# Kernel tuning notes

Measured on AMD Instinct MI355X. Metric: run time of the kernel, lower is better.

## Reference

```python
import jax, jax.numpy as jnp
import numpy as np
from jax import lax

NL, HID, DIN, DST, DCONV, DTR = 4, 256, 512, 16, 4, 16  # layers, d_model, expand*d_model, d_state, d_conv, dt_rank
B, H, W = 4, 256, 256


def setup_inputs() -> dict:
    key = jax.random.key(0)
    ks = jax.random.split(key, 8)
    def n(k, s, sc=0.02):
        return jax.random.normal(k, s, dtype=jnp.float32) * sc
    return {
        "x": jax.random.normal(ks[0], (B, 3, H, W), dtype=jnp.float32),
        "conv1_w": n(ks[1], (HID // 2, 3, 3, 3), 0.1), "conv1_b": jnp.zeros((HID // 2,), jnp.float32),
        "gn1_w": jnp.ones((HID // 2,), jnp.float32), "gn1_b": jnp.zeros((HID // 2,), jnp.float32),
        "conv2_w": n(ks[2], (HID, HID // 2, 3, 3), 0.05), "conv2_b": jnp.zeros((HID,), jnp.float32),
        "gn2_w": jnp.ones((HID,), jnp.float32), "gn2_b": jnp.zeros((HID,), jnp.float32),
        "ln_w": jnp.ones((NL, HID), jnp.float32), "ln_b": jnp.zeros((NL, HID), jnp.float32),
        "in_proj_w": n(ks[3], (NL, 2 * DIN, HID)),
        "conv1d_w": n(ks[4], (NL, DIN, 1, DCONV), 0.1), "conv1d_b": jnp.zeros((NL, DIN), jnp.float32),
        "x_proj_w": n(ks[5], (NL, DTR + 2 * DST, DIN)),
        "dt_proj_w": n(ks[6], (NL, DIN, DTR), 0.1),
        "dt_proj_b": jnp.full((NL, DIN), -4.6, dtype=jnp.float32),  # softplus(-4.6) ~ 0.01
        "A_log": jnp.broadcast_to(jnp.log(jnp.arange(1, DST + 1, dtype=jnp.float32)), (NL, DIN, DST)) + jnp.zeros((NL, DIN, DST), jnp.float32),
        "D": jnp.ones((NL, DIN), jnp.float32),
        "out_proj_w": n(ks[7], (NL, HID, DIN)),
    }


def conv2d_s2(x, w, b):
    y = lax.conv_general_dilated(x, w, (2, 2), [(1, 1), (1, 1)],
                                 dimension_numbers=('NCHW', 'OIHW', 'NCHW'))
    return y + b[None, :, None, None]


def group_norm(x, w, b, groups=8, eps=1e-5):
    Bb, C, Hh, Ww = x.shape
    xg = x.reshape(Bb, groups, C // groups, Hh, Ww)
    m = xg.mean((2, 3, 4), keepdims=True)
    v = xg.var((2, 3, 4), keepdims=True)
    xg = (xg - m) * lax.rsqrt(v + eps)
    return xg.reshape(Bb, C, Hh, Ww) * w[None, :, None, None] + b[None, :, None, None]


def layer_norm(x, w, b, eps=1e-5):
    m = x.mean(-1, keepdims=True)
    v = x.var(-1, keepdims=True)
    return (x - m) * lax.rsqrt(v + eps) * w + b


def mamba(x, ipw, cw, cb, xpw, dpw, dpb, A_log, Dp, opw):
    # x: [B, L, HID]
    Bb, L, _ = x.shape
    xz = jnp.einsum('bld,ed->ble', x, ipw)           # [B, L, 2*DIN]
    xc, z = jnp.split(xz, 2, axis=-1)
    # depthwise causal conv1d over L
    u = xc.transpose(0, 2, 1)                        # [B, DIN, L]
    u = lax.conv_general_dilated(u, cw, (1,), [(DCONV - 1, 0)],
                                 dimension_numbers=('NCH', 'OIH', 'NCH'),
                                 feature_group_count=DIN)
    xc = jax.nn.silu(u + cb[None, :, None]).transpose(0, 2, 1)  # [B, L, DIN]
    x_dbl = jnp.einsum('bld,ed->ble', xc, xpw)       # [B, L, DTR+2*DST]
    dt, Bm, Cm = jnp.split(x_dbl, [DTR, DTR + DST], axis=-1)
    delta = jax.nn.softplus(jnp.einsum('blr,dr->bld', dt, dpw) + dpb)  # [B, L, DIN]
    A = -jnp.exp(A_log)                              # [DIN, DST]
    dA = jnp.exp(jnp.einsum('bld,dn->bldn', delta, A))
    dBu = jnp.einsum('bld,bln,bld->bldn', delta, Bm, xc)

    def step(h, inp):
        dA_t, dBu_t, C_t = inp
        h = dA_t * h + dBu_t                         # [B, DIN, DST]
        return h, jnp.einsum('bdn,bn->bd', h, C_t)

    h0 = jnp.zeros((Bb, DIN, DST), x.dtype)
    _, ys = lax.scan(step, h0, (dA.transpose(1, 0, 2, 3), dBu.transpose(1, 0, 2, 3), Cm.transpose(1, 0, 2)))
    y = ys.transpose(1, 0, 2) + xc * Dp              # [B, L, DIN]
    y = y * jax.nn.silu(z)
    return jnp.einsum('bld,ed->ble', y, opw)         # [B, L, HID]


def reference(x, conv1_w, conv1_b, gn1_w, gn1_b, conv2_w, conv2_b, gn2_w, gn2_b,
              ln_w, ln_b, in_proj_w, conv1d_w, conv1d_b, x_proj_w, dt_proj_w,
              dt_proj_b, A_log, D, out_proj_w):
    y = jax.nn.silu(group_norm(conv2d_s2(x, conv1_w, conv1_b), gn1_w, gn1_b))
    y = jax.nn.silu(group_norm(conv2d_s2(y, conv2_w, conv2_b), gn2_w, gn2_b))
    Bb, C, h, w = y.shape
    s = y.reshape(Bb, C, h * w).transpose(0, 2, 1)   # b (h w) c
    for i in range(NL):
        s = s + mamba(layer_norm(s, ln_w[i], ln_b[i]), in_proj_w[i], conv1d_w[i],
                      conv1d_b[i], x_proj_w[i], dt_proj_w[i], dt_proj_b[i],
                      A_log[i], D[i], out_proj_w[i])
    return (s, h, w)
```

## Files before the change

### kernel.cpp

```cpp
#include <hip/hip_runtime.h>
#include <math.h>

#define BB 4
#define C1 128
#define H1 128
#define W1 128
#define C2 256
#define H2 64
#define W2 64
#define LSEQ 4096
#define HID 256
#define DIN 512
#define DST 16
#define DTR 16
#define NL 4
#define NCHUNK 128
#define LCH 32

typedef unsigned short u16;
using short8 = __attribute__((ext_vector_type(8))) short;
using f32x4  = __attribute__((ext_vector_type(4))) float;
using f32x2  = __attribute__((ext_vector_type(2))) float;

static __device__ __forceinline__ float dsilu(float x){
    return x / (1.0f + __expf(-x));
}
static __device__ __forceinline__ u16 f2bf(float f){
    unsigned u = __float_as_uint(f);
    u += 0x7FFF + ((u >> 16) & 1);
    return (u16)(u >> 16);
}
static __device__ __forceinline__ float bf2f(u16 v){
    return __uint_as_float(((unsigned)v) << 16);
}

#define GLL16(g, l) __builtin_amdgcn_global_load_lds( \
    (const __attribute__((address_space(1))) void*)(g), \
    (__attribute__((address_space(3))) void*)(l), 16, 0, 0)

__global__ void f2bf_kernel(const float* __restrict__ src, u16* __restrict__ dst){
    int idx = blockIdx.x * 256 + threadIdx.x;
    dst[idx] = f2bf(src[idx]);
}
__global__ void wdt_prep_kernel(const float* __restrict__ xpw, const float* __restrict__ dpw,
                                u16* __restrict__ wcomb){
    int idx = blockIdx.x * 256 + threadIdx.x;
    int k = idx & 511;
    int n = (idx >> 9) % 640;
    int layer = idx / (640*512);
    u16 val = 0;
    if(n < 512){
        const float* dp = dpw + ((long)layer*512 + n)*16;
        const float* xp = xpw + (long)layer*48*512 + k;
        float acc = 0.f;
        #pragma unroll
        for(int r = 0; r < 16; ++r) acc = fmaf(dp[r], xp[(long)r*512], acc);
        val = f2bf(acc);
    } else if(n < 544){
        int row = n - 512 + 16;
        val = f2bf(xpw[((long)layer*48 + row)*512 + k]);
    }
    wcomb[((long)layer*640 + n)*512 + k] = val;
}
__global__ void c2w_prep_kernel(const float* __restrict__ src, u16* __restrict__ dst){
    int idx = blockIdx.x * 256 + threadIdx.x;
    int ci = idx & 127, p = (idx >> 7) % 9, co = idx / (9*128);
    int kh = p / 3, kw = p - 3*kh;
    dst[idx] = f2bf(src[((co*128 + ci)*3 + kh)*3 + kw]);
}
__global__ void xt_zero_kernel(unsigned* __restrict__ xt){
    xt[blockIdx.x * 256 + threadIdx.x] = 0;
}

__global__ __launch_bounds__(256) void conv1_kernel(
        const float* __restrict__ x, const float* __restrict__ w,
        const float* __restrict__ bias, float* __restrict__ y){
    __shared__ float xs[9][260];
    int oh = blockIdx.x, b = blockIdx.y;
    int tid = threadIdx.x;
    #pragma unroll
    for(int r = 0; r < 9; ++r){
        int ci = r / 3, kh = r - 3*ci;
        int ih = 2*oh - 1 + kh;
        float v = 0.f;
        if(ih >= 0) v = x[((b*3 + ci)*256 + ih)*256 + tid];
        xs[r][tid + 1] = v;
        if(tid == 0) xs[r][0] = 0.f;
    }
    __syncthreads();
    int co = tid >> 1, h = tid & 1;
    float wr[27];
    #pragma unroll
    for(int j = 0; j < 27; ++j) wr[j] = w[co*27 + j];
    float bz = bias[co];
    long obase = ((long)((b*128 + co)*128 + oh))*128 + h*64;
    #pragma unroll 4
    for(int i = 0; i < 64; ++i){
        int iw0 = 2*(h*64 + i);
        float acc = bz;
        #pragma unroll
        for(int r = 0; r < 9; ++r){
            acc = fmaf(xs[r][iw0+0], wr[r*3+0], acc);
            acc = fmaf(xs[r][iw0+1], wr[r*3+1], acc);
            acc = fmaf(xs[r][iw0+2], wr[r*3+2], acc);
        }
        y[obase + i] = acc;
    }
}

__global__ void zero_stats_kernel(float* __restrict__ stats){
    stats[threadIdx.x] = 0.0f;
}

__global__ void gn_stats_kernel(const float* __restrict__ x, float* __restrict__ stats,
                                int elems_per_group){
    const int EPB = 16384;
    long base = (long)blockIdx.x * EPB;
    int g = (int)(base / elems_per_group);
    float s = 0.f, ss = 0.f;
    for(int j = threadIdx.x; j < EPB; j += 256){
        float v = x[base + j];
        s += v; ss += v*v;
    }
    #pragma unroll
    for(int off = 32; off; off >>= 1){
        s  += __shfl_down(s,  off);
        ss += __shfl_down(ss, off);
    }
    __shared__ float ls[4], lss[4];
    int wid = threadIdx.x >> 6, lane = threadIdx.x & 63;
    if(lane == 0){ ls[wid] = s; lss[wid] = ss; }
    __syncthreads();
    if(threadIdx.x == 0){
        atomicAdd(&stats[g],      ls[0]+ls[1]+ls[2]+ls[3]);
        atomicAdd(&stats[32+g], lss[0]+lss[1]+lss[2]+lss[3]);
    }
}

__global__ void gn1_transform_kernel(const float* __restrict__ y1, const float* __restrict__ stats,
                                     const float* __restrict__ w, const float* __restrict__ bias,
                                     u16* __restrict__ xt){
    __shared__ float tile[32][33];
    int b = blockIdx.z >> 7, ih = blockIdx.z & 127;
    int c0 = blockIdx.y * 32, w0 = blockIdx.x * 32;
    int tx = threadIdx.x, ty = threadIdx.y;
    const float cnt = 16.f * 128.f * 128.f;
    #pragma unroll
    for(int i = 0; i < 4; ++i){
        int ci = c0 + ty + i*8;
        int g = b*8 + (ci >> 4);
        float mean = stats[g] / cnt;
        float var  = stats[32+g] / cnt - mean*mean;
        float rstd = rsqrtf(var + 1e-5f);
        float v = y1[(((long)(b*C1 + ci))*H1 + ih)*W1 + w0 + tx];
        tile[ty + i*8][tx] = dsilu((v - mean) * rstd * w[ci] + bias[ci]);
    }
    __syncthreads();
    #pragma unroll
    for(int i = 0; i < 4; ++i){
        int iwl = ty + i*8;
        xt[((long)(b*130 + ih + 1)*130 + (w0 + iwl + 1))*128 + c0 + tx] = f2bf(tile[tx][iwl]);
    }
}

__global__ __launch_bounds__(256) void conv2gemm_bf16_kernel(
        const u16* __restrict__ xt, const u16* __restrict__ w2,
        const float* __restrict__ bias, float* __restrict__ y2t){
    __shared__ u16 Asm[128*32];
    __shared__ u16 Bsm[128*32];
    int m0 = blockIdx.x * 128, n0 = blockIdx.y * 128;
    int tid = threadIdx.x;
    long abase[2]; const u16* bbase[2];
    #pragma unroll
    for(int it = 0; it < 2; ++it){
        int c = it*256 + tid;
        int r = c >> 2, q = (c & 3) * 8;
        int m = m0 + r;
        int b = m >> 12, oh = (m >> 6) & 63, ow = m & 63;
        abase[it] = ((long)(b*130 + 2*oh)*130 + 2*ow)*128 + q;
        bbase[it] = w2 + (long)(n0 + r)*1152 + q;
    }
    int wave = tid >> 6, lane = tid & 63;
    int wr = wave >> 1, wc = wave & 1;
    int lm = lane & 15, lq = lane >> 4;
    f32x4 acc[4][4] = {};
    #pragma unroll 1
    for(int p = 0; p < 9; ++p){
        int kh = p / 3, kw = p - 3*kh;
        int aoff = (kh*130 + kw)*128;
        #pragma unroll 1
        for(int ci0 = 0; ci0 < 128; ci0 += 32){
            #pragma unroll
            for(int it = 0; it < 2; ++it){
                int c = it*256 + tid;
                GLL16(xt + abase[it] + aoff + ci0, &Asm[c*8]);
                GLL16(bbase[it] + p*128 + ci0, &Bsm[c*8]);
            }
            __syncthreads();
            short8 af[4], bf[4];
            #pragma unroll
            for(int i = 0; i < 4; ++i){
                af[i] = *(const short8*)&Asm[(wr*64 + i*16 + lm)*32 + lq*8];
                bf[i] = *(const short8*)&Bsm[(wc*64 + i*16 + lm)*32 + lq*8];
            }
            #pragma unroll
            for(int i = 0; i < 4; ++i)
                #pragma unroll
                for(int j = 0; j < 4; ++j)
                    acc[i][j] = __builtin_amdgcn_mfma_f32_16x16x32_bf16(af[i], bf[j], acc[i][j], 0, 0, 0);
            __syncthreads();
        }
    }
    #pragma unroll
    for(int i = 0; i < 4; ++i){
        long row = m0 + wr*64 + i*16 + lq*4;
        #pragma unroll
        for(int j = 0; j < 4; ++j){
            int col = n0 + wc*64 + j*16 + lm;
            float bz = bias[col];
            #pragma unroll
            for(int r = 0; r < 4; ++r)
                y2t[(row + r)*256L + col] = acc[i][j][r] + bz;
        }
    }
}

__global__ void gn2t_stats_kernel(const float* __restrict__ y2t, float* __restrict__ stats){
    int b = blockIdx.y;
    long row0 = (long)b*LSEQ + blockIdx.x*64;
    int c = threadIdx.x;
    float s = 0.f, ss = 0.f;
    for(int r = 0; r < 64; ++r){
        float v = y2t[(row0 + r)*C2 + c];
        s += v; ss += v*v;
    }
    #pragma unroll
    for(int off = 16; off; off >>= 1){
        s  += __shfl_down(s,  off);
        ss += __shfl_down(ss, off);
    }
    if((c & 31) == 0){
        int g = b*8 + (c >> 5);
        atomicAdd(&stats[g], s);
        atomicAdd(&stats[32+g], ss);
    }
}

__global__ void gn2t_apply_ln_kernel(const float* __restrict__ y2t, const float* __restrict__ stats,
                                     const float* __restrict__ gw, const float* __restrict__ gb,
                                     const float* __restrict__ lw, const float* __restrict__ lb,
                                     float* __restrict__ s, u16* __restrict__ xln){
    long row = blockIdx.x;
    int c = threadIdx.x;
    int b = (int)(row >> 12);
    int g = b*8 + (c >> 5);
    const float cnt = 32.f * (float)LSEQ;
    float mean = stats[g] / cnt;
    float var  = stats[32+g] / cnt - mean*mean;
    float rstd = rsqrtf(var + 1e-5f);
    float v = dsilu((y2t[row*HID + c] - mean) * rstd * gw[c] + gb[c]);
    s[row*HID + c] = v;
    float sm = v, sq = v*v;
    #pragma unroll
    for(int off = 32; off; off >>= 1){
        sm += __shfl_down(sm, off);
        sq += __shfl_down(sq, off);
    }
    __shared__ float pa[4], pb[4], res[2];
    int wid = c >> 6, lane = c & 63;
    if(lane == 0){ pa[wid] = sm; pb[wid] = sq; }
    __syncthreads();
    if(c == 0){
        float t  = pa[0]+pa[1]+pa[2]+pa[3];
        float tt = pb[0]+pb[1]+pb[2]+pb[3];
        float m2 = t / 256.f;
        float v2 = tt / 256.f - m2*m2;
        res[0] = m2; res[1] = rsqrtf(v2 + 1e-5f);
    }
    __syncthreads();
    xln[row*HID + c] = f2bf((v - res[0]) * res[1] * lw[c] + lb[c]);
}

__global__ __launch_bounds__(256) void gemm_bf16_kernel(
        const u16* __restrict__ A, const u16* __restrict__ B, void* __restrict__ Cv,
        int K, int Nact, int ldc, int mode){
    __shared__ u16 Asm[128*32];
    __shared__ u16 Bsm[128*32];
    int m0 = blockIdx.x * 128, n0 = blockIdx.y * 128;
    int tid = threadIdx.x;
    int wave = tid >> 6, lane = tid & 63;
    int wr = wave >> 1, wc = wave & 1;
    int lm = lane & 15, lq = lane >> 4;
    f32x4 acc[4][4] = {};
    for(int k0 = 0; k0 < K; k0 += 32){
        #pragma unroll
        for(int it = 0; it < 2; ++it){
            int c = it*256 + tid;
            int row = c >> 2, kq = (c & 3) * 8;
            GLL16(A + (long)(m0 + row)*K + k0 + kq, &Asm[c*8]);
            GLL16(B + (long)(n0 + row)*K + k0 + kq, &Bsm[c*8]);
        }
        __syncthreads();
        short8 af[4], bf[4];
        #pragma unroll
        for(int i = 0; i < 4; ++i){
            af[i] = *(const short8*)&Asm[(wr*64 + i*16 + lm)*32 + lq*8];
            bf[i] = *(const short8*)&Bsm[(wc*64 + i*16 + lm)*32 + lq*8];
        }
        #pragma unroll
        for(int i = 0; i < 4; ++i)
            #pragma unroll
            for(int j = 0; j < 4; ++j)
                acc[i][j] = __builtin_amdgcn_mfma_f32_16x16x32_bf16(af[i], bf[j], acc[i][j], 0, 0, 0);
        __syncthreads();
    }
    #pragma unroll
    for(int i = 0; i < 4; ++i){
        long row = m0 + wr*64 + i*16 + lq*4;
        #pragma unroll
        for(int j = 0; j < 4; ++j){
            int col = n0 + wc*64 + j*16 + lm;
            if(col < Nact){
                #pragma unroll
                for(int r = 0; r < 4; ++r){
                    long idx = (row + r)*(long)ldc + col;
                    if(mode == 2) ((u16*)Cv)[idx] = f2bf(acc[i][j][r]);
                    else          ((float*)Cv)[idx] = acc[i][j][r];
                }
            }
        }
    }
}

__global__ __launch_bounds__(256) void gemm_dtbc_kernel(
        const u16* __restrict__ A, const u16* __restrict__ B,
        const float* __restrict__ dpb, u16* __restrict__ dv,
        float* __restrict__ xdbl32){
    __shared__ u16 Asm[128*32];
    __shared__ u16 Bsm[128*32];
    int m0 = blockIdx.x * 128, n0 = blockIdx.y * 128;
    int tid = threadIdx.x;
    int wave = tid >> 6, lane = tid & 63;
    int wr = wave >> 1, wc = wave & 1;
    int lm = lane & 15, lq = lane >> 4;
    f32x4 acc[4][4] = {};
    for(int k0 = 0; k0 < 512; k0 += 32){
        #pragma unroll
        for(int it = 0; it < 2; ++it){
            int c = it*256 + tid;
            int row = c >> 2, kq = (c & 3) * 8;
            GLL16(A + (long)(m0 + row)*512 + k0 + kq, &Asm[c*8]);
            GLL16(B + (long)(n0 + row)*512 + k0 + kq, &Bsm[c*8]);
        }
        __syncthreads();
        short8 af[4], bf[4];
        #pragma unroll
        for(int i = 0; i < 4; ++i){
            af[i] = *(const short8*)&Asm[(wr*64 + i*16 + lm)*32 + lq*8];
            bf[i] = *(const short8*)&Bsm[(wc*64 + i*16 + lm)*32 + lq*8];
        }
        #pragma unroll
        for(int i = 0; i < 4; ++i)
            #pragma unroll
            for(int j = 0; j < 4; ++j)
                acc[i][j] = __builtin_amdgcn_mfma_f32_16x16x32_bf16(af[i], bf[j], acc[i][j], 0, 0, 0);
        __syncthreads();
    }
    if(n0 < 512){
        #pragma unroll
        for(int i = 0; i < 4; ++i){
            long row = m0 + wr*64 + i*16 + lq*4;
            #pragma unroll
            for(int j = 0; j < 4; ++j){
                int col = n0 + wc*64 + j*16 + lm;
                float bz = dpb[col];
                #pragma unroll
                for(int r = 0; r < 4; ++r){
                    float v = acc[i][j][r] + bz;
                    v = (v > 20.f) ? v : __logf(1.f + __expf(v));
                    dv[(row + r)*512L + col] = f2bf(v);
                }
            }
        }
    } else {
        #pragma unroll
        for(int i = 0; i < 4; ++i){
            long row = m0 + wr*64 + i*16 + lq*4;
            #pragma unroll
            for(int j = 0; j < 4; ++j){
                int lcol = wc*64 + j*16 + lm;
                if(lcol < 32){
                    #pragma unroll
                    for(int r = 0; r < 4; ++r)
                        xdbl32[(row + r)*32L + lcol] = acc[i][j][r];
                }
            }
        }
    }
}

__global__ __launch_bounds__(256) void gemm_out_ln_kernel(
        const u16* __restrict__ A, const u16* __restrict__ B,
        float* __restrict__ s, u16* __restrict__ xln,
        const float* __restrict__ lw, const float* __restrict__ lb){
    __shared__ u16 Asm[64*32];
    __shared__ u16 Bsm[256*32];
    int m0 = blockIdx.x * 64;
    int tid = threadIdx.x;
    int w = tid >> 6, lane = tid & 63;
    int lm = lane & 15, lq = lane >> 4;
    f32x4 acc[16] = {};
    for(int k0 = 0; k0 < 512; k0 += 32){
        {
            int row = tid >> 2, kq = (tid & 3) * 8;
            GLL16(A + (long)(m0 + row)*512 + k0 + kq, &Asm[tid*8]);
        }
        #pragma unroll
        for(int it = 0; it < 4; ++it){
            int c = it*256 + tid;
            int row = c >> 2, kq = (c & 3) * 8;
            GLL16(B + (long)row*512 + k0 + kq, &Bsm[c*8]);
        }
        __syncthreads();
        short8 af = *(const short8*)&Asm[(w*16 + lm)*32 + lq*8];
        #pragma unroll
        for(int j = 0; j < 16; ++j){
            short8 bf = *(const short8*)&Bsm[(j*16 + lm)*32 + lq*8];
            acc[j] = __builtin_amdgcn_mfma_f32_16x16x32_bf16(af, bf, acc[j], 0, 0, 0);
        }
        __syncthreads();
    }
    int row0 = m0 + w*16 + lq*4;
    float psum[4] = {0.f,0.f,0.f,0.f}, psq[4] = {0.f,0.f,0.f,0.f};
    #pragma unroll
    for(int j = 0; j < 16; ++j){
        int col = j*16 + lm;
        #pragma unroll
        for(int r = 0; r < 4; ++r){
            long idx = (long)(row0 + r)*HID + col;
            float v = s[idx] + acc[j][r];
            acc[j][r] = v;
            s[idx] = v;
            psum[r] += v; psq[r] += v*v;
        }
    }
    #pragma unroll
    for(int mask = 1; mask <= 8; mask <<= 1){
        #pragma unroll
        for(int r = 0; r < 4; ++r){
            psum[r] += __shfl_xor(psum[r], mask);
            psq[r]  += __shfl_xor(psq[r],  mask);
        }
    }
    float mean[4], rstd[4];
    #pragma unroll
    for(int r = 0; r < 4; ++r){
        mean[r] = psum[r] * (1.f/256.f);
        float var = psq[r] * (1.f/256.f) - mean[r]*mean[r];
        rstd[r] = rsqrtf(var + 1e-5f);
    }
    #pragma unroll
    for(int j = 0; j < 16; ++j){
        int col = j*16 + lm;
        float wv = lw[col], bv = lb[col];
        #pragma unroll
        for(int r = 0; r < 4; ++r){
            long idx = (long)(row0 + r)*HID + col;
            xln[idx] = f2bf((acc[j][r] - mean[r]) * rstd[r] * wv + bv);
        }
    }
}

__global__ void conv1d_silu_kernel(const u16* __restrict__ xz, const float* __restrict__ w,
                                   const float* __restrict__ bias, u16* __restrict__ xcv){
    int idx = blockIdx.x * 256 + threadIdx.x;
    int e = idx * 8;
    int d0 = e & 511;
    long m = e >> 9;
    int l = (int)(m & 4095);
    short8 xrow[4];
    const u16* xp = xz + m*(2*DIN) + d0;
    #pragma unroll
    for(int j = 0; j < 4; ++j){
        int t = l - 3 + j;
        if(t >= 0) xrow[j] = *(const short8*)(xp + (long)(j-3)*(2*DIN));
        else       xrow[j] = (short8){0,0,0,0,0,0,0,0};
    }
    float wv[8][4];
    #pragma unroll
    for(int k = 0; k < 8; k += 2){
        float4 a = *(const float4*)(w + (d0+k)*4);
        float4 b = *(const float4*)(w + (d0+k+1)*4);
        wv[k][0]=a.x; wv[k][1]=a.y; wv[k][2]=a.z; wv[k][3]=a.w;
        wv[k+1][0]=b.x; wv[k+1][1]=b.y; wv[k+1][2]=b.z; wv[k+1][3]=b.w;
    }
    float bz[8];
    {
        float4 a = *(const float4*)(bias + d0);
        float4 b = *(const float4*)(bias + d0 + 4);
        bz[0]=a.x; bz[1]=a.y; bz[2]=a.z; bz[3]=a.w;
        bz[4]=b.x; bz[5]=b.y; bz[6]=b.z; bz[7]=b.w;
    }
    short8 out;
    #pragma unroll
    for(int k = 0; k < 8; ++k){
        float acc = bz[k];
        #pragma unroll
        for(int j = 0; j < 4; ++j)
            acc = fmaf(bf2f((u16)xrow[j][k]), wv[k][j], acc);
        out[k] = (short)f2bf(dsilu(acc));
    }
    *(short8*)(xcv + m*DIN + d0) = out;
}

__global__ __launch_bounds__(256) void scan1_kernel(
        const u16* __restrict__ xcvb, const u16* __restrict__ dvin,
        const float* __restrict__ xdbl32, const float* __restrict__ Alog,
        float* __restrict__ aprod, float* __restrict__ hend){
    int d = blockIdx.y * 256 + threadIdx.x;
    int c = blockIdx.x;
    int b = blockIdx.z;
    __shared__ float bm[LCH][16];
    {
        int t = threadIdx.x >> 4, n = threadIdx.x & 15;
        #pragma unroll
        for(int it = 0; it < 2; ++it){
            long p = ((long)(b*LSEQ + c*LCH + t + it*16))*32;
            bm[t + it*16][n] = xdbl32[p + n];
        }
    }
    __syncthreads();
    float An[16];
    #pragma unroll
    for(int n = 0; n < 16; ++n)
        An[n] = -__expf(Alog[d*16 + n]);
    float An0 = An[0];
    bool structural = true;
    #pragma unroll
    for(int n = 0; n < 16; ++n)
        structural = structural && (fabsf(An[n] - (float)(n+1)*An0) <= 1e-3f*(float)(n+1));
    long base = ((long)(b*LSEQ + c*LCH))*DIN + d;
    long ob = (((long)(b*NCHUNK + c))*DIN + d)*16;
    if(structural){
        f32x2 h2[8];
        #pragma unroll
        for(int i = 0; i < 8; ++i) h2[i] = (f32x2){0.f, 0.f};
        float sumdv = 0.f;
        float xv_n = bf2f(xcvb[base]);
        float dv_n = bf2f(dvin[base]);
        for(int t = 0; t < LCH; ++t){
            float xv = xv_n, dv = dv_n;
            if(t + 1 < LCH){
                xv_n = bf2f(xcvb[base + (long)(t+1)*DIN]);
                dv_n = bf2f(dvin[base + (long)(t+1)*DIN]);
            }
            sumdv += dv;
            float db = dv * xv;
            float r1 = __expf(dv * An0);
            float r2 = r1 * r1;
            f32x2 rr = {r2, r2};
            f32x2 e2[8];
            e2[0] = (f32x2){r1, r2};
            #pragma unroll
            for(int i = 1; i < 8; ++i) e2[i] = e2[i-1] * rr;
            f32x2 db2 = {db, db};
            const f32x2* b2 = (const f32x2*)&bm[t][0];
            #pragma unroll
            for(int i = 0; i < 8; ++i) h2[i] = e2[i]*h2[i] + db2*b2[i];
        }
        float R = __expf(An0 * sumdv);
        float Rp = R;
        const float* hp = (const float*)h2;
        #pragma unroll
        for(int n = 0; n < 16; ++n){
            aprod[ob+n] = Rp; Rp *= R;
            hend[ob+n] = hp[n];
        }
    } else {
        float h[16], ap[16];
        #pragma unroll
        for(int n = 0; n < 16; ++n){ h[n] = 0.f; ap[n] = 1.f; }
        for(int t = 0; t < LCH; ++t){
            float dv = bf2f(dvin[base + (long)t*DIN]);
            float db = dv * bf2f(xcvb[base + (long)t*DIN]);
            #pragma unroll
            for(int n = 0; n < 16; ++n){
                float e = __expf(dv * An[n]);
                ap[n] *= e;
                h[n] = fmaf(e, h[n], db * bm[t][n]);
            }
        }
        #pragma unroll
        for(int n = 0; n < 16; ++n){ aprod[ob+n] = ap[n]; hend[ob+n] = h[n]; }
    }
}

__global__ void scan2_kernel(const float* __restrict__ aprod, const float* __restrict__ hend,
                             float* __restrict__ hinit){
    int idx = blockIdx.x * 256 + threadIdx.x;
    int n = idx & 15, d = (idx >> 4) & 511, b = idx >> 13;
    const long stride = (long)DIN * 16;
    long p0 = (((long)(b*NCHUNK))*DIN + d)*16 + n;
    float h = 0.f;
    for(int c = 0; c < NCHUNK; c += 8){
        float a[8], e[8];
        #pragma unroll
        for(int j = 0; j < 8; ++j){
            long p = p0 + (long)(c + j)*stride;
            a[j] = aprod[p]; e[j] = hend[p];
        }
        #pragma unroll
        for(int j = 0; j < 8; ++j){
            hinit[p0 + (long)(c + j)*stride] = h;
            h = fmaf(a[j], h, e[j]);
        }
    }
}

__global__ __launch_bounds__(256) void scan3_kernel(
        const u16* __restrict__ xcvb, const u16* __restrict__ dvin,
        const float* __restrict__ xdbl32, const float* __restrict__ Alog,
        const float* __restrict__ hinit, const float* __restrict__ Dp,
        const u16* __restrict__ xz, u16* __restrict__ yout){
    int d = blockIdx.y * 256 + threadIdx.x;
    int c = blockIdx.x;
    int b = blockIdx.z;
    __shared__ float bm[LCH][16], cm[LCH][16];
    {
        int t = threadIdx.x >> 4, n = threadIdx.x & 15;
        #pragma unroll
        for(int it = 0; it < 2; ++it){
            long p = ((long)(b*LSEQ + c*LCH + t + it*16))*32;
            bm[t + it*16][n] = xdbl32[p + n];
            cm[t + it*16][n] = xdbl32[p + 16 + n];
        }
    }
    __syncthreads();
    float An[16];
    long hb = (((long)(b*NCHUNK + c))*DIN + d)*16;
    #pragma unroll
    for(int n = 0; n < 16; ++n)
        An[n] = -__expf(Alog[d*16 + n]);
    float An0 = An[0];
    bool structural = true;
    #pragma unroll
    for(int n = 0; n < 16; ++n)
        structural = structural && (fabsf(An[n] - (float)(n+1)*An0) <= 1e-3f*(float)(n+1));
    float Dv = Dp[d];
    long base  = ((long)(b*LSEQ + c*LCH))*DIN + d;
    long zbase = ((long)(b*LSEQ + c*LCH))*(2*DIN) + DIN + d;
    if(structural){
        f32x2 h2[8];
        {
            const f32x2* hi = (const f32x2*)&hinit[hb];
            #pragma unroll
            for(int i = 0; i < 8; ++i) h2[i] = hi[i];
        }
        float xv_n = bf2f(xcvb[base]);
        float z_n  = bf2f(xz[zbase]);
        float dv_n = bf2f(dvin[base]);
        for(int t = 0; t < LCH; ++t){
            float xv = xv_n, z = z_n, dv = dv_n;
            if(t + 1 < LCH){
                xv_n = bf2f(xcvb[base + (long)(t+1)*DIN]);
                z_n  = bf2f(xz[zbase + (long)(t+1)*(2*DIN)]);
                dv_n = bf2f(dvin[base + (long)(t+1)*DIN]);
            }
            float db = dv * xv;
            float r1 = __expf(dv * An0);
            float r2 = r1 * r1;
            f32x2 rr = {r2, r2};
            f32x2 e2[8];
            e2[0] = (f32x2){r1, r2};
            #pragma unroll
            for(int i = 1; i < 8; ++i) e2[i] = e2[i-1] * rr;
            f32x2 db2 = {db, db};
            const f32x2* b2 = (const f32x2*)&bm[t][0];
            const f32x2* c2 = (const f32x2*)&cm[t][0];
            f32x2 y2 = {0.f, 0.f};
            #pragma unroll
            for(int i = 0; i < 8; ++i){
                h2[i] = e2[i]*h2[i] + db2*b2[i];
                y2 = y2 + h2[i]*c2[i];
            }
            float y = y2[0] + y2[1];
            y = fmaf(xv, Dv, y);
            yout[base + (long)t*DIN] = f2bf(y * dsilu(z));
        }
    } else {
        float h[16];
        #pragma unroll
        for(int n = 0; n < 16; ++n) h[n] = hinit[hb + n];
        for(int t = 0; t < LCH; ++t){
            float dv = bf2f(dvin[base + (long)t*DIN]);
            float xv = bf2f(xcvb[base + (long)t*DIN]);
            float db = dv * xv;
            float y = 0.f;
            #pragma unroll
            for(int n = 0; n < 16; ++n){
                float e = __expf(dv * An[n]);
                h[n] = fmaf(e, h[n], db * bm[t][n]);
                y = fmaf(h[n], cm[t][n], y);
            }
            y = fmaf(xv, Dv, y);
            float z = bf2f(xz[zbase + (long)t*(2*DIN)]);
            yout[base + (long)t*DIN] = f2bf(y * dsilu(z));
        }
    }
}

__global__ void copyout_kernel(const float* __restrict__ s, float* __restrict__ out, int out_size){
    int idx = blockIdx.x * 256 + threadIdx.x;
    if(idx >= out_size) return;
    out[idx] = (idx < BB*LSEQ*HID) ? s[idx] : 64.0f;
}

extern "C" void kernel_launch(void* const* d_in, const int* in_sizes, int n_in,
                              void* d_out, int out_size, void* d_ws, size_t ws_size,
                              hipStream_t stream){
    const float* x        = (const float*)d_in[0];
    const float* conv1_w  = (const float*)d_in[1];
    const float* conv1_b  = (const float*)d_in[2];
    const float* gn1_w    = (const float*)d_in[3];
    const float* gn1_b    = (const float*)d_in[4];
    const float* conv2_w  = (const float*)d_in[5];
    const float* conv2_b  = (const float*)d_in[6];
    const float* gn2_w    = (const float*)d_in[7];
    const float* gn2_b    = (const float*)d_in[8];
    const float* ln_w     = (const float*)d_in[9];
    const float* ln_b     = (const float*)d_in[10];
    const float* in_proj  = (const float*)d_in[11];
    const float* c1d_w    = (const float*)d_in[12];
    const float* c1d_b    = (const float*)d_in[13];
    const float* x_proj   = (const float*)d_in[14];
    const float* dt_w     = (const float*)d_in[15];
    const float* dt_b     = (const float*)d_in[16];
    const float* A_log    = (const float*)d_in[17];
    const float* Dvec     = (const float*)d_in[18];
    const float* out_proj = (const float*)d_in[19];

    float* ws = (float*)d_ws;
    float* s      = ws;
    u16*   xz_bf  = (u16*)(ws + 4194304);
    float* y1     = ws + 4194304;
    u16*   xt     = (u16*)(ws + 12582912);
    u16*   xcv_bf = (u16*)(ws + 16909312);
    float* y2t    = ws + 16909312;
    u16*   xln_bf = (u16*)(ws + 21103616);
    float* xdbl   = ws + 23200768;
    float* aprod  = ws + 23987200;
    float* hendb  = ws + 28181504;
    u16*   y_bf   = (u16*)aprod;
    float* hinit  = ws + 32375808;
    float* stats  = ws + 36570112;
    u16*   ipw_bf = (u16*)(ws + 36570176);
    u16*   opw_bf = ipw_bf + 1048576;
    u16*   c2w_bf = opw_bf + 524288;
    u16*   dv_bf  = (u16*)(ws + 37635200);
    u16*   wcomb  = (u16*)(ws + 41829504);

    f2bf_kernel<<<4096, 256, 0, stream>>>(in_proj, ipw_bf);
    f2bf_kernel<<<2048, 256, 0, stream>>>(out_proj, opw_bf);
    c2w_prep_kernel<<<1152, 256, 0, stream>>>(conv2_w, c2w_bf);
    wdt_prep_kernel<<<5120, 256, 0, stream>>>(x_proj, dt_w, wcomb);

    conv1_kernel<<<dim3(128,4), 256, 0, stream>>>(x, conv1_w, conv1_b, y1);
    zero_stats_kernel<<<1, 64, 0, stream>>>(stats);
    gn_stats_kernel<<<512, 256, 0, stream>>>(y1, stats, 16*H1*W1);
    xt_zero_kernel<<<16900, 256, 0, stream>>>((unsigned*)xt);
    gn1_transform_kernel<<<dim3(4,4,512), dim3(32,8), 0, stream>>>(y1, stats, gn1_w, gn1_b, xt);
    conv2gemm_bf16_kernel<<<dim3(128,2), 256, 0, stream>>>(xt, c2w_bf, conv2_b, y2t);
    zero_stats_kernel<<<1, 64, 0, stream>>>(stats);
    gn2t_stats_kernel<<<dim3(64,4), 256, 0, stream>>>(y2t, stats);
    gn2t_apply_ln_kernel<<<16384, 256, 0, stream>>>(y2t, stats, gn2_w, gn2_b,
                                                    ln_w, ln_b, s, xln_bf);

    for(int layer = 0; layer < NL; ++layer){
        const float* cw  = c1d_w + (long)layer*DIN*4;
        const float* cb  = c1d_b + (long)layer*DIN;
        const float* dpb = dt_b  + (long)layer*DIN;
        const float* Al  = A_log + (long)layer*DIN*DST;
        const float* Dl  = Dvec  + (long)layer*DIN;
        int lnext = (layer + 1) & 3;

        gemm_bf16_kernel<<<dim3(128,8), 256, 0, stream>>>(
            xln_bf, ipw_bf + (long)layer*1024*256, xz_bf, HID, 2*DIN, 2*DIN, 2);
        conv1d_silu_kernel<<<4096, 256, 0, stream>>>(xz_bf, cw, cb, xcv_bf);
        gemm_dtbc_kernel<<<dim3(128,5), 256, 0, stream>>>(
            xcv_bf, wcomb + (long)layer*640*512, dpb, dv_bf, xdbl);
        scan1_kernel<<<dim3(NCHUNK,2,BB), 256, 0, stream>>>(
            xcv_bf, dv_bf, xdbl, Al, aprod, hendb);
        scan2_kernel<<<128, 256, 0, stream>>>(aprod, hendb, hinit);
        scan3_kernel<<<dim3(NCHUNK,2,BB), 256, 0, stream>>>(
            xcv_bf, dv_bf, xdbl, Al, hinit, Dl, xz_bf, y_bf);
        gemm_out_ln_kernel<<<256, 256, 0, stream>>>(
            y_bf, opw_bf + (long)layer*256*512, s, xln_bf,
            ln_w + lnext*HID, ln_b + lnext*HID);
    }

    copyout_kernel<<<(out_size + 255)/256, 256, 0, stream>>>(s, (float*)d_out, out_size);
}
```

Measured before the change: 864.7 us.

## Double-buffer LDS tiles with async prefetch and XOR-swizzle in all bf16 GEMMs

Converts the four MFMA GEMM kernels (conv2 implicit GEMM, generic GEMM, dt/BC GEMM, out-proj+LN GEMM) to double-buffered LDS. The next K-tile is issued through global_load_lds while the current tile is consumed, using explicit vmcnt waits and raw barriers. It also XOR-swizzles the 16-byte chunk placement within each row to cut LDS bank conflicts on the short8 fragment reads. The cost is twice the shared memory per block, which may lower occupancy, plus reliance on hand-placed waitcnt correctness.

New measurement: 845.2 us. 1.02x faster.

```diff
diff --git a/kernel.cpp b/kernel.cpp
--- a/kernel.cpp
+++ b/kernel.cpp
@@ -38,6 +38,16 @@
     (const __attribute__((address_space(1))) void*)(g), \
     (__attribute__((address_space(3))) void*)(l), 16, 0, 0)
 
+#define VMW4 asm volatile("s_waitcnt vmcnt(4)" ::: "memory")
+#define VMW5 asm volatile("s_waitcnt vmcnt(5)" ::: "memory")
+#define VMW0 asm volatile("s_waitcnt vmcnt(0)" ::: "memory")
+
+static __device__ __forceinline__ void blockbar(){
+    asm volatile("" ::: "memory");
+    __builtin_amdgcn_s_barrier();
+    asm volatile("" ::: "memory");
+}
+
 __global__ void f2bf_kernel(const float* __restrict__ src, u16* __restrict__ dst){
     int idx = blockIdx.x * 256 + threadIdx.x;
     dst[idx] = f2bf(src[idx]);
@@ -166,50 +176,63 @@
 __global__ __launch_bounds__(256) void conv2gemm_bf16_kernel(
         const u16* __restrict__ xt, const u16* __restrict__ w2,
         const float* __restrict__ bias, float* __restrict__ y2t){
-    __shared__ u16 Asm[128*32];
-    __shared__ u16 Bsm[128*32];
+    __shared__ u16 Asm[2][128*32];
+    __shared__ u16 Bsm[2][128*32];
     int m0 = blockIdx.x * 128, n0 = blockIdx.y * 128;
     int tid = threadIdx.x;
-    long abase[2]; const u16* bbase[2];
+    long abase[2]; const u16* bbase[2]; int ldst[2];
     #pragma unroll
     for(int it = 0; it < 2; ++it){
         int c = it*256 + tid;
-        int r = c >> 2, q = (c & 3) * 8;
+        int r = c >> 2;
+        int kq = ((c & 3) ^ ((r >> 1) & 3)) * 8;
         int m = m0 + r;
         int b = m >> 12, oh = (m >> 6) & 63, ow = m & 63;
-        abase[it] = ((long)(b*130 + 2*oh)*130 + 2*ow)*128 + q;
-        bbase[it] = w2 + (long)(n0 + r)*1152 + q;
+        abase[it] = ((long)(b*130 + 2*oh)*130 + 2*ow)*128 + kq;
+        bbase[it] = w2 + (long)(n0 + r)*1152 + kq;
+        ldst[it] = c*8;
     }
     int wave = tid >> 6, lane = tid & 63;
     int wr = wave >> 1, wc = wave & 1;
     int lm = lane & 15, lq = lane >> 4;
+    int swq = (lq ^ ((lm >> 1) & 3)) * 8;
     f32x4 acc[4][4] = {};
-    #pragma unroll 1
-    for(int p = 0; p < 9; ++p){
-        int kh = p / 3, kw = p - 3*kh;
-        int aoff = (kh*130 + kw)*128;
-        #pragma unroll 1
-        for(int ci0 = 0; ci0 < 128; ci0 += 32){
+    #pragma unroll
+    for(int it = 0; it < 2; ++it){
+        GLL16(xt + abase[it], &Asm[0][ldst[it]]);
+        GLL16(bbase[it], &Bsm[0][ldst[it]]);
+    }
+    for(int kk = 0; kk < 36; ++kk){
+        int cur = kk & 1;
+        if(kk + 1 < 36){
+            int k2 = kk + 1;
+            int p = k2 >> 2, cs = k2 & 3;
+            int kh = p / 3, kw = p - 3*kh;
+            int ao = (kh*130 + kw)*128 + cs*32;
+            int bo = k2*32;
             #pragma unroll
             for(int it = 0; it < 2; ++it){
-                int c = it*256 + tid;
-                GLL16(xt + abase[it] + aoff + ci0, &Asm[c*8]);
-                GLL16(bbase[it] + p*128 + ci0, &Bsm[c*8]);
-            }
-            __syncthreads();
-            short8 af[4], bf[4];
-            #pragma unroll
-            for(int i = 0; i < 4; ++i){
-                af[i] = *(const short8*)&Asm[(wr*64 + i*16 + lm)*32 + lq*8];
-                bf[i] = *(const short8*)&Bsm[(wc*64 + i*16 + lm)*32 + lq*8];
-            }
-            #pragma unroll
-            for(int i = 0; i < 4; ++i)
-                #pragma unroll
-                for(int j = 0; j < 4; ++j)
-                    acc[i][j] = __builtin_amdgcn_mfma_f32_16x16x32_bf16(af[i], bf[j], acc[i][j], 0, 0, 0);
-            __syncthreads();
-        }
+                GLL16(xt + abase[it] + ao, &Asm[cur^1][ldst[it]]);
+                GLL16(bbase[it] + bo, &Bsm[cur^1][ldst[it]]);
+            }
+            VMW4;
+        } else {
+            VMW0;
+        }
+        blockbar();
+        short8 af[4], bf[4];
+        #pragma unroll
+        for(int i = 0; i < 4; ++i){
+            af[i] = *(const short8*)&Asm[cur][(wr*64 + i*16 + lm)*32 + swq];
+            bf[i] = *(const short8*)&Bsm[cur][(wc*64 + i*16 + lm)*32 + swq];
+        }
+        #pragma unroll
+        for(int i = 0; i < 4; ++i)
+            #pragma unroll
+            for(int j = 0; j < 4; ++j)
+                acc[i][j] = __builtin_amdgcn_mfma_f32_16x16x32_bf16(af[i], bf[j], acc[i][j], 0, 0, 0);
+        __builtin_amdgcn_sched_barrier(0);
+        blockbar();
     }
     #pragma unroll
     for(int i = 0; i < 4; ++i){
@@ -284,35 +307,58 @@
 __global__ __launch_bounds__(256) void gemm_bf16_kernel(
         const u16* __restrict__ A, const u16* __restrict__ B, void* __restrict__ Cv,
         int K, int Nact, int ldc, int mode){
-    __shared__ u16 Asm[128*32];
-    __shared__ u16 Bsm[128*32];
+    __shared__ u16 Asm[2][128*32];
+    __shared__ u16 Bsm[2][128*32];
     int m0 = blockIdx.x * 128, n0 = blockIdx.y * 128;
     int tid = threadIdx.x;
     int wave = tid >> 6, lane = tid & 63;
     int wr = wave >> 1, wc = wave & 1;
     int lm = lane & 15, lq = lane >> 4;
+    int swq = (lq ^ ((lm >> 1) & 3)) * 8;
+    const u16* ag[2]; const u16* bg[2]; int ldst[2];
+    #pragma unroll
+    for(int it = 0; it < 2; ++it){
+        int c = it*256 + tid;
+        int r = c >> 2;
+        int kq = ((c & 3) ^ ((r >> 1) & 3)) * 8;
+        ag[it] = A + (long)(m0 + r)*K + kq;
+        bg[it] = B + (long)(n0 + r)*K + kq;
+        ldst[it] = c*8;
+    }
     f32x4 acc[4][4] = {};
-    for(int k0 = 0; k0 < K; k0 += 32){
-        #pragma unroll
-        for(int it = 0; it < 2; ++it){
-            int c = it*256 + tid;
-            int row = c >> 2, kq = (c & 3) * 8;
-            GLL16(A + (long)(m0 + row)*K + k0 + kq, &Asm[c*8]);
-            GLL16(B + (long)(n0 + row)*K + k0 + kq, &Bsm[c*8]);
-        }
-        __syncthreads();
+    int nk = K >> 5;
+    #pragma unroll
+    for(int it = 0; it < 2; ++it){
+        GLL16(ag[it], &Asm[0][ldst[it]]);
+        GLL16(bg[it], &Bsm[0][ldst[it]]);
+    }
+    for(int kt = 0; kt < nk; ++kt){
+        int cur = kt & 1;
+        if(kt + 1 < nk){
+            int ko = (kt + 1) << 5;
+            #pragma unroll
+            for(int it = 0; it < 2; ++it){
+                GLL16(ag[it] + ko, &Asm[cur^1][ldst[it]]);
+                GLL16(bg[it] + ko, &Bsm[cur^1][ldst[it]]);
+            }
+            VMW4;
+        } else {
+            VMW0;
+        }
+        blockbar();
         short8 af[4], bf[4];
         #pragma unroll
         for(int i = 0; i < 4; ++i){
-            af[i] = *(const short8*)&Asm[(wr*64 + i*16 + lm)*32 + lq*8];
-            bf[i] = *(const short8*)&Bsm[(wc*64 + i*16 + lm)*32 + lq*8];
+            af[i] = *(const short8*)&Asm[cur][(wr*64 + i*16 + lm)*32 + swq];
+            bf[i] = *(const short8*)&Bsm[cur][(wc*64 + i*16 + lm)*32 + swq];
         }
         #pragma unroll
         for(int i = 0; i < 4; ++i)
             #pragma unroll
             for(int j = 0; j < 4; ++j)
                 acc[i][j] = __builtin_amdgcn_mfma_f32_16x16x32_bf16(af[i], bf[j], acc[i][j], 0, 0, 0);
-        __syncthreads();
+        __builtin_amdgcn_sched_barrier(0);
+        blockbar();
     }
     #pragma unroll
     for(int i = 0; i < 4; ++i){
@@ -336,35 +382,57 @@
         const u16* __restrict__ A, const u16* __restrict__ B,
         const float* __restrict__ dpb, u16* __restrict__ dv,
         float* __restrict__ xdbl32){
-    __shared__ u16 Asm[128*32];
-    __shared__ u16 Bsm[128*32];
+    __shared__ u16 Asm[2][128*32];
+    __shared__ u16 Bsm[2][128*32];
     int m0 = blockIdx.x * 128, n0 = blockIdx.y * 128;
     int tid = threadIdx.x;
     int wave = tid >> 6, lane = tid & 63;
     int wr = wave >> 1, wc = wave & 1;
     int lm = lane & 15, lq = lane >> 4;
+    int swq = (lq ^ ((lm >> 1) & 3)) * 8;
+    const u16* ag[2]; const u16* bg[2]; int ldst[2];
+    #pragma unroll
+    for(int it = 0; it < 2; ++it){
+        int c = it*256 + tid;
+        int r = c >> 2;
+        int kq = ((c & 3) ^ ((r >> 1) & 3)) * 8;
+        ag[it] = A + (long)(m0 + r)*512 + kq;
+        bg[it] = B + (long)(n0 + r)*512 + kq;
+        ldst[it] = c*8;
+    }
     f32x4 acc[4][4] = {};
-    for(int k0 = 0; k0 < 512; k0 += 32){
-        #pragma unroll
-        for(int it = 0; it < 2; ++it){
-            int c = it*256 + tid;
-            int row = c >> 2, kq = (c & 3) * 8;
-            GLL16(A + (long)(m0 + row)*512 + k0 + kq, &Asm[c*8]);
-            GLL16(B + (long)(n0 + row)*512 + k0 + kq, &Bsm[c*8]);
-        }
-        __syncthreads();
+    #pragma unroll
+    for(int it = 0; it < 2; ++it){
+        GLL16(ag[it], &Asm[0][ldst[it]]);
+        GLL16(bg[it], &Bsm[0][ldst[it]]);
+    }
+    for(int kt = 0; kt < 16; ++kt){
+        int cur = kt & 1;
+        if(kt + 1 < 16){
+            int ko = (kt + 1) << 5;
+            #pragma unroll
+            for(int it = 0; it < 2; ++it){
+                GLL16(ag[it] + ko, &Asm[cur^1][ldst[it]]);
+                GLL16(bg[it] + ko, &Bsm[cur^1][ldst[it]]);
+            }
+            VMW4;
+        } else {
+            VMW0;
+        }
+        blockbar();
         short8 af[4], bf[4];
         #pragma unroll
         for(int i = 0; i < 4; ++i){
-            af[i] = *(const short8*)&Asm[(wr*64 + i*16 + lm)*32 + lq*8];
-            bf[i] = *(const short8*)&Bsm[(wc*64 + i*16 + lm)*32 + lq*8];
+            af[i] = *(const short8*)&Asm[cur][(wr*64 + i*16 + lm)*32 + swq];
+            bf[i] = *(const short8*)&Bsm[cur][(wc*64 + i*16 + lm)*32 + swq];
         }
         #pragma unroll
         for(int i = 0; i < 4; ++i)
             #pragma unroll
             for(int j = 0; j < 4; ++j)
                 acc[i][j] = __builtin_amdgcn_mfma_f32_16x16x32_bf16(af[i], bf[j], acc[i][j], 0, 0, 0);
-        __syncthreads();
+        __builtin_amdgcn_sched_barrier(0);
+        blockbar();
     }
     if(n0 < 512){
         #pragma unroll
@@ -403,32 +471,52 @@
         const u16* __restrict__ A, const u16* __restrict__ B,
         float* __restrict__ s, u16* __restrict__ xln,
         const float* __restrict__ lw, const float* __restrict__ lb){
-    __shared__ u16 Asm[64*32];
-    __shared__ u16 Bsm[256*32];
+    __shared__ u16 Asm[2][64*32];
+    __shared__ u16 Bsm[2][256*32];
     int m0 = blockIdx.x * 64;
     int tid = threadIdx.x;
     int w = tid >> 6, lane = tid & 63;
     int lm = lane & 15, lq = lane >> 4;
+    int swq = (lq ^ ((lm >> 1) & 3)) * 8;
+    int ra = tid >> 2;
+    int kqa = ((tid & 3) ^ ((ra >> 1) & 3)) * 8;
+    const u16* agA = A + (long)(m0 + ra)*512 + kqa;
+    int lda = tid*8;
+    const u16* bg[4]; int ldb[4];
+    #pragma unroll
+    for(int it = 0; it < 4; ++it){
+        int c = it*256 + tid;
+        int r = c >> 2;
+        int kq = ((c & 3) ^ ((r >> 1) & 3)) * 8;
+        bg[it] = B + (long)r*512 + kq;
+        ldb[it] = c*8;
+    }
     f32x4 acc[16] = {};
-    for(int k0 = 0; k0 < 512; k0 += 32){
-        {
-            int row = tid >> 2, kq = (tid & 3) * 8;
-            GLL16(A + (long)(m0 + row)*512 + k0 + kq, &Asm[tid*8]);
-        }
-        #pragma unroll
-        for(int it = 0; it < 4; ++it){
-            int c = it*256 + tid;
-            int row = c >> 2, kq = (c & 3) * 8;
-            GLL16(B + (long)row*512 + k0 + kq, &Bsm[c*8]);
-        }
-        __syncthreads();
-        short8 af = *(const short8*)&Asm[(w*16 + lm)*32 + lq*8];
+    GLL16(agA, &Asm[0][lda]);
+    #pragma unroll
+    for(int it = 0; it < 4; ++it)
+        GLL16(bg[it], &Bsm[0][ldb[it]]);
+    for(int kt = 0; kt < 16; ++kt){
+        int cur = kt & 1;
+        if(kt + 1 < 16){
+            int ko = (kt + 1) << 5;
+            GLL16(agA + ko, &Asm[cur^1][lda]);
+            #pragma unroll
+            for(int it = 0; it < 4; ++it)
+                GLL16(bg[it] + ko, &Bsm[cur^1][ldb[it]]);
+            VMW5;
+        } else {
+            VMW0;
+        }
+        blockbar();
+        short8 af = *(const short8*)&Asm[cur][(w*16 + lm)*32 + swq];
         #pragma unroll
         for(int j = 0; j < 16; ++j){
-            short8 bf = *(const short8*)&Bsm[(j*16 + lm)*32 + lq*8];
+            short8 bf = *(const short8*)&Bsm[cur][(j*16 + lm)*32 + swq];
             acc[j] = __builtin_amdgcn_mfma_f32_16x16x32_bf16(af, bf, acc[j], 0, 0, 0);
         }
-        __syncthreads();
+        __builtin_amdgcn_sched_barrier(0);
+        blockbar();
     }
     int row0 = m0 + w*16 + lq*4;
     float psum[4] = {0.f,0.f,0.f,0.f}, psq[4] = {0.f,0.f,0.f,0.f};
```
